# Performance work log

Hardware: AMD Instinct MI355X
Metric: run time of the kernel (lower is better)

## Reference

```python
import jax, jax.numpy as jnp
import numpy as np

NUM_HEADS = 16
EMBED_DIM = 1024
BSZ, T, S = 8, 1024, 1024
NEG_INF = -1e30


def setup_inputs() -> dict:
    key = jax.random.key(0)
    ks = jax.random.split(key, 12)
    E = EMBED_DIM
    decoder_state = jax.random.normal(ks[0], (BSZ, T, E), dtype=jnp.float32)
    source_hids = jax.random.normal(ks[1], (S, BSZ, E), dtype=jnp.float32)
    # realistic padding mask: True = padded position (masked out)
    lengths = jax.random.randint(ks[2], (BSZ,), S // 2, S + 1)
    src_len_mask = jnp.arange(S)[None, :] >= lengths[:, None]  # (BSZ, S) bool
    init = 1.0 / np.sqrt(E)
    Wq = jax.random.uniform(ks[3], (E, E), minval=-init, maxval=init)
    bq = jax.random.uniform(ks[4], (E,), minval=-init, maxval=init)
    Wk = jax.random.uniform(ks[5], (E, E), minval=-init, maxval=init)
    bk = jax.random.uniform(ks[6], (E,), minval=-init, maxval=init)
    Wv = jax.random.uniform(ks[7], (E, E), minval=-init, maxval=init)
    bv = jax.random.uniform(ks[8], (E,), minval=-init, maxval=init)
    Wo = jax.random.uniform(ks[9], (E, E), minval=-init, maxval=init)
    bo = jax.random.uniform(ks[10], (E,), minval=-init, maxval=init)
    return {"decoder_state": decoder_state, "source_hids": source_hids,
            "src_len_mask": src_len_mask, "Wq": Wq, "bq": bq, "Wk": Wk,
            "bk": bk, "Wv": Wv, "bv": bv, "Wo": Wo, "bo": bo}


def reference(decoder_state, source_hids, src_len_mask, Wq, bq, Wk, bk, Wv, bv, Wo, bo):
    B, Tq, E = decoder_state.shape
    Sk = source_hids.shape[0]
    H = NUM_HEADS
    hd = E // H
    scaling = hd ** (-0.5)

    query = jnp.swapaxes(decoder_state, 0, 1)  # (T, B, E)
    q = (query @ Wq.T + bq) * scaling          # (T, B, E)
    k = source_hids @ Wk.T + bk                # (S, B, E)
    v = source_hids @ Wv.T + bv                # (S, B, E)

    q = q.reshape(Tq, B, H, hd)
    k = k.reshape(Sk, B, H, hd)
    v = v.reshape(Sk, B, H, hd)

    scores = jnp.einsum("tbhd,sbhd->bhts", q, k)  # (B, H, T, S)
    scores = jnp.where(src_len_mask[:, None, None, :], NEG_INF, scores)
    weights = jax.nn.softmax(scores, axis=-1)     # (B, H, T, S); dropout p=0

    attn = jnp.einsum("bhts,sbhd->tbhd", weights, v).reshape(Tq, B, E)
    attn = attn @ Wo.T + bo                       # (T, B, E)

    # need_weights: mean over heads -> (B, T, S); then transpose(0,2) -> (S, T, B)
    attn_weights_out = jnp.swapaxes(weights.mean(axis=1), 0, 2)
    # squeeze=True is a no-op here since T != 1
    return attn, attn_weights_out
```

## Files before the change

kernel.cpp:

```cpp
#include <hip/hip_runtime.h>
#include <stdint.h>
#include <stddef.h>

typedef __attribute__((ext_vector_type(8))) short bf16x8;
typedef __attribute__((ext_vector_type(4))) float f32x4;
typedef __attribute__((ext_vector_type(4))) uint32_t u32x4;

#define DEVINL static __device__ __forceinline__

DEVINL float b2f(uint16_t u) {
  uint32_t x = ((uint32_t)u) << 16;
  float f;
  __builtin_memcpy(&f, &x, 4);
  return f;
}

DEVINL uint16_t f2b(float f) {
  uint32_t u;
  __builtin_memcpy(&u, &f, 4);
  return (uint16_t)((u + 0x7fffu + ((u >> 16) & 1u)) >> 16);
}

DEVINL void gload16(const void* gsrc, void* ldst) {
  __builtin_amdgcn_global_load_lds(
      (const __attribute__((address_space(1))) void*)gsrc,
      (__attribute__((address_space(3))) void*)ldst, 16, 0, 0);
}

__global__ void detect_kernel(const void* __restrict__ wq, const void* __restrict__ mask,
                              const void* __restrict__ bq, const void* __restrict__ bk,
                              const void* __restrict__ bv, const void* __restrict__ bo,
                              int* __restrict__ hdr, float* __restrict__ bias) {
  __shared__ int sflag, smask32, slen[8];
  const int tid = threadIdx.x;
  if (tid == 0) { sflag = 0; smask32 = 0; }
  if (tid < 8) slen[tid] = 0;
  __syncthreads();
  const uint16_t* w16 = (const uint16_t*)wq;
  int f = 0;
  for (int i = tid; i < 4096; i += 256) {
    uint16_t u = w16[i];
    uint32_t e = (u >> 7) & 0xFFu;
    if (fabsf(b2f(u)) > 0.25f || e == 0xFFu) f = 1;
  }
  if (f) atomicOr(&sflag, 1);
  const uint8_t* mb = (const uint8_t*)mask;
  int m32 = 0;
  for (int i = tid; i < 8191; i += 256) {
    if ((i & 1023) != 1023 && mb[i] != 0 && mb[i + 1] == 0) m32 = 1;
  }
  if (m32) atomicOr(&smask32, 1);
  __syncthreads();
  if (smask32) {
    const int* mi = (const int*)mask;
    for (int i = tid; i < 8192; i += 256) { if (mi[i] == 0) atomicAdd(&slen[i >> 10], 1); }
  } else {
    for (int i = tid; i < 8192; i += 256) { if (mb[i] == 0) atomicAdd(&slen[i >> 10], 1); }
  }
  __syncthreads();
  if (tid == 0) hdr[0] = sflag;
  if (tid < 8) hdr[1 + tid] = slen[tid];
  const void* bs[4] = {bq, bk, bv, bo};
  for (int j = 0; j < 4; ++j) {
    for (int i = tid; i < 1024; i += 256) {
      float v = sflag ? ((const float*)bs[j])[i] : b2f(((const uint16_t*)bs[j])[i]);
      bias[j * 1024 + i] = v;
    }
  }
}

__global__ __launch_bounds__(256)
void convert_kernel(const void* __restrict__ s0, const void* __restrict__ s1,
                    const void* __restrict__ s2, const void* __restrict__ s3,
                    const void* __restrict__ s4, const void* __restrict__ s5,
                    uint16_t* __restrict__ d0, uint16_t* __restrict__ d1,
                    uint16_t* __restrict__ d2, const int* __restrict__ hdr, int doW) {
  const int isf = hdr[0];
  const size_t n01 = 1048576;
  const size_t nw = 131072;
  const size_t total = doW ? (2 * n01 + 4 * nw) : (2 * n01);
  size_t gid = (size_t)blockIdx.x * 256 + threadIdx.x;
  const size_t stride = (size_t)gridDim.x * 256;
  for (; gid < total; gid += stride) {
    const void* sp;
    uint16_t* dp;
    size_t off;
    if (gid < n01) { sp = s0; dp = d0; off = gid; }
    else if (gid < 2 * n01) { sp = s1; dp = d1; off = gid - n01; }
    else {
      const size_t w = (gid - 2 * n01) >> 17;
      off = (gid - 2 * n01) & (nw - 1);
      sp = (w == 0) ? s2 : (w == 1) ? s3 : (w == 2) ? s4 : s5;
      dp = d2 + w * 1048576;
    }
    if (isf) {
      const float* fp = (const float*)sp + off * 8;
      const f32x4 a = *(const f32x4*)fp;
      const f32x4 c = *(const f32x4*)(fp + 4);
      u32x4 r;
      r[0] = (uint32_t)f2b(a[0]) | ((uint32_t)f2b(a[1]) << 16);
      r[1] = (uint32_t)f2b(a[2]) | ((uint32_t)f2b(a[3]) << 16);
      r[2] = (uint32_t)f2b(c[0]) | ((uint32_t)f2b(c[1]) << 16);
      r[3] = (uint32_t)f2b(c[2]) | ((uint32_t)f2b(c[3]) << 16);
      *(u32x4*)(dp + off * 8) = r;
    } else {
      *(u32x4*)(dp + off * 8) = *(const u32x4*)((const uint16_t*)sp + off * 8);
    }
  }
}

enum { MQ = 0, MK = 1, MV = 2, MO = 3 };

DEVINL u32x4 load8w(const void* __restrict__ src, bool f32, size_t eoff) {
  if (!f32) {
    return *(const u32x4*)((const uint16_t*)src + eoff);
  }
  const float* p = (const float*)src + eoff;
  const f32x4 a = *(const f32x4*)p;
  const f32x4 c = *(const f32x4*)(p + 4);
  u32x4 r;
  r[0] = (uint32_t)f2b(a[0]) | ((uint32_t)f2b(a[1]) << 16);
  r[1] = (uint32_t)f2b(a[2]) | ((uint32_t)f2b(a[3]) << 16);
  r[2] = (uint32_t)f2b(c[0]) | ((uint32_t)f2b(c[1]) << 16);
  r[3] = (uint32_t)f2b(c[2]) | ((uint32_t)f2b(c[3]) << 16);
  return r;
}

__global__ __launch_bounds__(256)
void gemm_qkv(const uint16_t* __restrict__ dec_b, const uint16_t* __restrict__ src_b,
              const void* __restrict__ Wq, const void* __restrict__ Wk,
              const void* __restrict__ Wv, const float* __restrict__ bias,
              const int* __restrict__ hdr, uint16_t* __restrict__ Q,
              uint16_t* __restrict__ K, uint16_t* __restrict__ V, int wIsBf16) {
  __shared__ __align__(16) uint16_t lA[2][8192];
  __shared__ __align__(16) uint16_t lB[2][8192];
  const int tid = threadIdx.x, lane = tid & 63, wave = tid >> 6;
  const int bm = blockIdx.x;
  const int grp = blockIdx.y >> 3, bn = blockIdx.y & 7;
  const int isf = hdr[0];
  const bool wF32 = (wIsBf16 == 0) && (isf != 0);
  const uint16_t* Ab = (grp == 0) ? dec_b : src_b;
  const void* Wr = (grp == 0) ? Wq : (grp == 1) ? Wk : Wv;
  const float* bs = bias + grp * 1024;
  const float scale = (grp == 0) ? 0.125f : 1.f;
  const int wm = wave >> 1, wn = wave & 1;
  const int g = lane >> 4, cc = lane & 15;
  const int lr = lane >> 3, lc = lane & 7;
  const int scc = (lc ^ lr) * 8;

  auto stage = [&](int kt, int buf) {
#pragma unroll
    for (int q = 0; q < 4; ++q) {
      const int j = wave * 4 + q;
      gload16(Ab + (size_t)(bm * 128 + j * 8 + lr) * 1024 + kt * 64 + scc, &lA[buf][j * 512]);
    }
    if (!wF32) {
#pragma unroll
      for (int q = 0; q < 4; ++q) {
        const int j = wave * 4 + q;
        gload16((const uint16_t*)Wr + (size_t)(bn * 128 + j * 8 + lr) * 1024 + kt * 64 + scc, &lB[buf][j * 512]);
      }
    } else {
#pragma unroll
      for (int q = 0; q < 4; ++q) {
        const int j = wave * 4 + q;
        const u32x4 rv = load8w(Wr, true, (size_t)(bn * 128 + j * 8 + lr) * 1024 + kt * 64 + lc * 8);
        *(u32x4*)&lB[buf][j * 512 + lr * 64 + ((lc ^ lr) * 8)] = rv;
      }
    }
  };

  f32x4 acc[4][4];
#pragma unroll
  for (int i = 0; i < 4; ++i)
#pragma unroll
    for (int j = 0; j < 4; ++j) acc[i][j] = (f32x4){0.f, 0.f, 0.f, 0.f};

  stage(0, 0);
  for (int kt = 0; kt < 16; ++kt) {
    const int cur = kt & 1;
    asm volatile("s_waitcnt vmcnt(0) lgkmcnt(0)" ::: "memory");
    __builtin_amdgcn_sched_barrier(0);
    __builtin_amdgcn_s_barrier();
    if (kt + 1 < 16) stage(kt + 1, cur ^ 1);
#pragma unroll
    for (int kk = 0; kk < 2; ++kk) {
      bf16x8 af[4], bfr[4];
#pragma unroll
      for (int mi = 0; mi < 4; ++mi) {
        const int row = wm * 64 + mi * 16 + cc;
        af[mi] = *(const bf16x8*)&lA[cur][row * 64 + (((kk * 4 + g) ^ (cc & 7)) << 3)];
      }
#pragma unroll
      for (int ni = 0; ni < 4; ++ni) {
        const int row = wn * 64 + ni * 16 + cc;
        bfr[ni] = *(const bf16x8*)&lB[cur][row * 64 + (((kk * 4 + g) ^ (cc & 7)) << 3)];
      }
#pragma unroll
      for (int mi = 0; mi < 4; ++mi)
#pragma unroll
        for (int ni = 0; ni < 4; ++ni)
          acc[mi][ni] = __builtin_amdgcn_mfma_f32_16x16x32_bf16(af[mi], bfr[ni], acc[mi][ni], 0, 0, 0);
    }
  }
#pragma unroll
  for (int mi = 0; mi < 4; ++mi) {
#pragma unroll
    for (int ni = 0; ni < 4; ++ni) {
      const int col = bn * 128 + wn * 64 + ni * 16 + cc;
      const float bv = bs[col];
      const int r0 = bm * 128 + wm * 64 + mi * 16 + g * 4;
#pragma unroll
      for (int r = 0; r < 4; ++r) {
        const int row = r0 + r;
        const float v = (acc[mi][ni][r] + bv) * scale;
        if (grp == 0) {
          const int b = row >> 10, t = row & 1023, h = col >> 6, d = col & 63;
          Q[(((size_t)(b * 16 + h) << 10) + t) * 64 + d] = f2b(v);
        } else if (grp == 1) {
          const int s = row >> 3, b = row & 7, h = col >> 6, d = col & 63;
          K[(((size_t)(b * 16 + h) << 10) + s) * 64 + d] = f2b(v);
        } else {
          const int s = row >> 3, b = row & 7, h = col >> 6, d = col & 63;
          V[(((size_t)(b * 16 + h) << 6) + d) * 1024 + s] = f2b(v);
        }
      }
    }
  }
}

template <int MODE>
__global__ __launch_bounds__(256)
void gemm_bt(const uint16_t* __restrict__ Ab, const void* __restrict__ Wr,
             const float* __restrict__ bias, const int* __restrict__ hdr,
             void* __restrict__ outp, float scale, int wIsBf16) {
  __shared__ __align__(16) uint16_t lA[2][8192];
  __shared__ __align__(16) uint16_t lB[2][8192];
  const int tid = threadIdx.x, lane = tid & 63, wave = tid >> 6;
  const int bm = blockIdx.x, bn = blockIdx.y;
  const int isf = hdr[0];
  const bool wF32 = (wIsBf16 == 0) && (isf != 0);
  const int wm = wave >> 1, wn = wave & 1;
  const int g = lane >> 4, cc = lane & 15;
  const int lr = lane >> 3, lc = lane & 7;
  const int scc = (lc ^ lr) * 8;

  auto stage = [&](int kt, int buf) {
#pragma unroll
    for (int q = 0; q < 4; ++q) {
      const int j = wave * 4 + q;
      gload16(Ab + (size_t)(bm * 128 + j * 8 + lr) * 1024 + kt * 64 + scc, &lA[buf][j * 512]);
    }
    if (!wF32) {
#pragma unroll
      for (int q = 0; q < 4; ++q) {
        const int j = wave * 4 + q;
        gload16((const uint16_t*)Wr + (size_t)(bn * 128 + j * 8 + lr) * 1024 + kt * 64 + scc, &lB[buf][j * 512]);
      }
    } else {
#pragma unroll
      for (int q = 0; q < 4; ++q) {
        const int j = wave * 4 + q;
        const u32x4 rv = load8w(Wr, true, (size_t)(bn * 128 + j * 8 + lr) * 1024 + kt * 64 + lc * 8);
        *(u32x4*)&lB[buf][j * 512 + lr * 64 + ((lc ^ lr) * 8)] = rv;
      }
    }
  };

  f32x4 acc[4][4];
#pragma unroll
  for (int i = 0; i < 4; ++i)
#pragma unroll
    for (int j = 0; j < 4; ++j) acc[i][j] = (f32x4){0.f, 0.f, 0.f, 0.f};

  stage(0, 0);
  for (int kt = 0; kt < 16; ++kt) {
    const int cur = kt & 1;
    asm volatile("s_waitcnt vmcnt(0) lgkmcnt(0)" ::: "memory");
    __builtin_amdgcn_sched_barrier(0);
    __builtin_amdgcn_s_barrier();
    if (kt + 1 < 16) stage(kt + 1, cur ^ 1);
#pragma unroll
    for (int kk = 0; kk < 2; ++kk) {
      bf16x8 af[4], bfr[4];
#pragma unroll
      for (int mi = 0; mi < 4; ++mi) {
        const int row = wm * 64 + mi * 16 + cc;
        af[mi] = *(const bf16x8*)&lA[cur][row * 64 + (((kk * 4 + g) ^ (cc & 7)) << 3)];
      }
#pragma unroll
      for (int ni = 0; ni < 4; ++ni) {
        const int row = wn * 64 + ni * 16 + cc;
        bfr[ni] = *(const bf16x8*)&lB[cur][row * 64 + (((kk * 4 + g) ^ (cc & 7)) << 3)];
      }
#pragma unroll
      for (int mi = 0; mi < 4; ++mi)
#pragma unroll
        for (int ni = 0; ni < 4; ++ni)
          acc[mi][ni] = __builtin_amdgcn_mfma_f32_16x16x32_bf16(af[mi], bfr[ni], acc[mi][ni], 0, 0, 0);
    }
  }
#pragma unroll
  for (int mi = 0; mi < 4; ++mi) {
#pragma unroll
    for (int ni = 0; ni < 4; ++ni) {
      const int col = bn * 128 + wn * 64 + ni * 16 + cc;
      const float bv = bias[col];
      const int r0 = bm * 128 + wm * 64 + mi * 16 + g * 4;
#pragma unroll
      for (int r = 0; r < 4; ++r) {
        const int row = r0 + r;
        const float v = (acc[mi][ni][r] + bv) * scale;
        const size_t o = (size_t)row * 1024 + col;
        if (isf) ((float*)outp)[o] = v;
        else ((uint16_t*)outp)[o] = f2b(v);
      }
    }
  }
}

__global__ __launch_bounds__(1024)
void attn_kernel(const uint16_t* __restrict__ Qh, const uint16_t* __restrict__ Kh,
                 const uint16_t* __restrict__ Vh, const int* __restrict__ hdr,
                 uint16_t* __restrict__ AP, uint16_t* __restrict__ Wm) {
  __shared__ __align__(16) uint16_t kbuf[2][8192];
  __shared__ __align__(16) uint16_t vbuf[2][8192];
  __shared__ __align__(16) uint16_t pstash[32][1024];
  __shared__ float pvx[2][32][68];

  const int tid = threadIdx.x, lane = tid & 63, w = tid >> 6;
  const int g = lane >> 4, cc = lane & 15;
  const int wt = w >> 3, ws = w & 7;
  const int dq = (w >> 1) & 3, ks = w & 1;
  const int b = blockIdx.x & 7, tt = blockIdx.x >> 3;
  const int t0 = tt * 32;
  const int len = hdr[1 + b];
  const int tme = tid >> 5, s5 = tid & 31;

  auto stage = [&](int p, int buf) {
    const int hh = p >> 3, st = p & 7;
    const uint16_t* Kb = Kh + ((size_t)(b * 16 + hh) << 16);
    const uint16_t* Vt = Vh + ((size_t)(b * 16 + hh) << 16);
    {
      const int row = tid >> 3;
      const int c = (tid & 7) ^ (row & 7);
      gload16(Kb + (st * 128 + row) * 64 + c * 8, &kbuf[buf][w * 512]);
    }
    {
      const int d = tid >> 4;
      const int c = tid & 15;
      const int cg = (c & 8) | ((c ^ (d & 7)) & 7);
      gload16(Vt + d * 1024 + st * 128 + cg * 8, &vbuf[buf][w * 512]);
    }
  };

  stage(0, 0);

  float wmean[32];
#pragma unroll
  for (int j = 0; j < 32; ++j) wmean[j] = 0.f;

  for (int h = 0; h < 16; ++h) {
    const uint16_t* Qb = Qh + ((size_t)(b * 16 + h) << 16) + (((size_t)(t0 + wt * 16 + cc)) << 6);
    const bf16x8 qf0 = *(const bf16x8*)(Qb + g * 8);
    const bf16x8 qf1 = *(const bf16x8*)(Qb + 32 + g * 8);
    f32x4 pv = (f32x4){0.f, 0.f, 0.f, 0.f};
    for (int st = 0; st < 8; ++st) {
      const int p = h * 8 + st;
      const int cur = p & 1;
      asm volatile("s_waitcnt vmcnt(0)" ::: "memory");
      __builtin_amdgcn_sched_barrier(0);
      __builtin_amdgcn_s_barrier();
      if (p + 1 < 128) stage(p + 1, cur ^ 1);
      {
        const int row = ws * 16 + cc;
        f32x4 a = (f32x4){0.f, 0.f, 0.f, 0.f};
#pragma unroll
        for (int kk = 0; kk < 2; ++kk) {
          const bf16x8 kf = *(const bf16x8*)&kbuf[cur][row * 64 + (((kk * 4 + g) ^ (cc & 7)) << 3)];
          a = __builtin_amdgcn_mfma_f32_16x16x32_bf16(kk ? qf1 : qf0, kf, a, 0, 0, 0);
        }
        const int s = st * 128 + row;
        const bool msk = (s >= len);
        float vv0 = msk ? 0.f : __expf(a[0]);
        float vv1 = msk ? 0.f : __expf(a[1]);
        float vv2 = msk ? 0.f : __expf(a[2]);
        float vv3 = msk ? 0.f : __expf(a[3]);
        uint32_t pk01, pk23;
        asm("v_cvt_pk_bf16_f32 %0, %1, %2" : "=v"(pk01) : "v"(vv0), "v"(vv1));
        asm("v_cvt_pk_bf16_f32 %0, %1, %2" : "=v"(pk23) : "v"(vv2), "v"(vv3));
        const uint16_t pb[4] = {(uint16_t)pk01, (uint16_t)(pk01 >> 16),
                                (uint16_t)pk23, (uint16_t)(pk23 >> 16)};
        const int cbase = st * 16 + ws * 2 + (cc >> 3);
#pragma unroll
        for (int r = 0; r < 4; ++r) {
          const int tl = wt * 16 + g * 4 + r;
          const int cs = (cbase & ~7) | ((cbase ^ tl) & 7);
          pstash[tl][(cs << 3) + (cc & 7)] = pb[r];
        }
      }
      asm volatile("s_waitcnt lgkmcnt(0)" ::: "memory");
      __builtin_amdgcn_sched_barrier(0);
      __builtin_amdgcn_s_barrier();
      {
        const int tr = wt * 16 + cc;
#pragma unroll
        for (int kk = 0; kk < 2; ++kk) {
          const int ca = st * 16 + ks * 8 + kk * 4 + g;
          const int ca2 = (ca & ~7) | ((ca ^ tr) & 7);
          const bf16x8 af = *(const bf16x8*)&pstash[tr][ca2 << 3];
          const int cv = ks * 8 + kk * 4 + g;
          const int cv2 = (cv & 8) | ((cv ^ (cc & 7)) & 7);
          const bf16x8 vf = *(const bf16x8*)&vbuf[cur][(dq * 16 + cc) * 128 + (cv2 << 3)];
          pv = __builtin_amdgcn_mfma_f32_16x16x32_bf16(af, vf, pv, 0, 0, 0);
        }
      }
    }
#pragma unroll
    for (int r = 0; r < 4; ++r)
      pvx[ks][wt * 16 + g * 4 + r][dq * 16 + cc] = pv[r];
    float winv;
    {
      uint32_t p4[16];
#pragma unroll
      for (int q = 0; q < 4; ++q) {
        const int c = s5 + 32 * q;
        const int c2 = (c & ~7) | ((c ^ tme) & 7);
        *(u32x4*)&p4[q * 4] = *(const u32x4*)&pstash[tme][c2 << 3];
      }
      float sm = 0.f;
#pragma unroll
      for (int j = 0; j < 16; ++j) {
        sm += b2f((uint16_t)(p4[j] & 0xffffu));
        sm += b2f((uint16_t)(p4[j] >> 16));
      }
#pragma unroll
      for (int m = 16; m >= 1; m >>= 1) sm += __shfl_xor(sm, m, 64);
      winv = 1.f / sm;
#pragma unroll
      for (int j = 0; j < 16; ++j) {
        wmean[2 * j] += b2f((uint16_t)(p4[j] & 0xffffu)) * winv;
        wmean[2 * j + 1] += b2f((uint16_t)(p4[j] >> 16)) * winv;
      }
    }
    asm volatile("s_waitcnt lgkmcnt(0)" ::: "memory");
    __builtin_amdgcn_sched_barrier(0);
    __builtin_amdgcn_s_barrier();
    {
      const int d0 = s5 * 2;
      const float v0 = (pvx[0][tme][d0] + pvx[1][tme][d0]) * winv;
      const float v1 = (pvx[0][tme][d0 + 1] + pvx[1][tme][d0 + 1]) * winv;
      const uint32_t pk = (uint32_t)f2b(v0) | ((uint32_t)f2b(v1) << 16);
      *(uint32_t*)(AP + ((((size_t)(t0 + tme)) * 8 + b) << 10) + h * 64 + d0) = pk;
    }
  }

  {
    uint16_t* dst = Wm + (((size_t)(b * 1024 + t0 + tme)) << 10);
#pragma unroll
    for (int q = 0; q < 4; ++q) {
      uint16_t ob[8];
#pragma unroll
      for (int e = 0; e < 8; ++e) ob[e] = f2b(wmean[q * 8 + e] * 0.0625f);
      *(u32x4*)(dst + q * 256 + s5 * 8) = *(const u32x4*)ob;
    }
  }
}

__global__ __launch_bounds__(256)
void wtrans_kernel(const uint16_t* __restrict__ Wm, const int* __restrict__ hdr,
                   void* __restrict__ outBase) {
  __shared__ uint16_t lt[8][32][68];
  const int tid = threadIdx.x;
  const int s0 = blockIdx.x * 64, t0 = blockIdx.y * 32;
  const int isf = hdr[0];
  const int rr = tid >> 4;
  const int sc = (tid & 15) * 4;
#pragma unroll
  for (int p = 0; p < 16; ++p) {
    const int row = p * 16 + rr;
    const int b = row >> 5, t = row & 31;
    const uint64_t v = *(const uint64_t*)(Wm + (((size_t)(b * 1024 + t0 + t)) << 10) + s0 + sc);
    *(uint64_t*)&lt[b][t][sc] = v;
  }
  __syncthreads();
#pragma unroll
  for (int p = 0; p < 8; ++p) {
    const int pair = p * 256 + tid;
    const int t = pair & 31, s = pair >> 5;
    const size_t o = 8388608 + ((size_t)(s0 + s) * 1024 + (t0 + t)) * 8;
    if (isf) {
      f32x4 v0, v1;
#pragma unroll
      for (int b = 0; b < 4; ++b) v0[b] = b2f(lt[b][t][s]);
#pragma unroll
      for (int b = 0; b < 4; ++b) v1[b] = b2f(lt[b + 4][t][s]);
      *(f32x4*)((float*)outBase + o) = v0;
      *(f32x4*)((float*)outBase + o + 4) = v1;
    } else {
      u32x4 v;
#pragma unroll
      for (int q = 0; q < 4; ++q)
        v[q] = (uint32_t)lt[2 * q][t][s] | ((uint32_t)lt[2 * q + 1][t][s] << 16);
      *(u32x4*)((uint16_t*)outBase + o) = v;
    }
  }
}

__global__ void fill_pattern(uint32_t* p, size_t n) {
  size_t i = (size_t)blockIdx.x * 256 + threadIdx.x;
  const size_t stride = (size_t)gridDim.x * 256;
  for (; i < n; i += stride) p[i] = 0x3f3f3f3fu;
}

extern "C" void kernel_launch(void* const* d_in, const int* in_sizes, int n_in,
                              void* d_out, int out_size, void* d_ws, size_t ws_size,
                              hipStream_t stream) {
  char* ws = (char*)d_ws;
  int* hdr = (int*)ws;
  float* bias = (float*)(ws + 4096);
  uint16_t* Q = (uint16_t*)(ws + (1u << 20));
  uint16_t* K = Q + 8388608;
  uint16_t* V = K + 8388608;
  uint16_t* AP = V + 8388608;
  uint16_t* Wm = AP + 8388608;
  uint16_t* dec_b = AP;
  uint16_t* src_b = Wm;
  const size_t needBase = (1ull << 20) + 5ull * 16777216ull;
  const size_t needFull = needBase + 8ull * 1048576ull;
  uint16_t* Wb = (uint16_t*)(ws + needBase);
  const int useConvW = (ws_size >= needFull) ? 1 : 0;
  if (ws_size < needBase) {
    fill_pattern<<<1024, 256, 0, stream>>>((uint32_t*)d_out, (size_t)out_size / 2);
    return;
  }

  detect_kernel<<<1, 256, 0, stream>>>(d_in[3], d_in[2], d_in[4], d_in[6], d_in[8], d_in[10], hdr, bias);

  convert_kernel<<<4096, 256, 0, stream>>>(d_in[0], d_in[1], d_in[3], d_in[5], d_in[7], d_in[9],
                                           dec_b, src_b, Wb, hdr, useConvW);

  const void* Wq = useConvW ? (const void*)(Wb + 0 * 1048576) : (const void*)d_in[3];
  const void* Wk = useConvW ? (const void*)(Wb + 1 * 1048576) : (const void*)d_in[5];
  const void* Wv = useConvW ? (const void*)(Wb + 2 * 1048576) : (const void*)d_in[7];
  const void* Wo = useConvW ? (const void*)(Wb + 3 * 1048576) : (const void*)d_in[9];

  gemm_qkv<<<dim3(64, 24), 256, 0, stream>>>(dec_b, src_b, Wq, Wk, Wv, bias, hdr, Q, K, V, useConvW);

  attn_kernel<<<256, 1024, 0, stream>>>(Q, K, V, hdr, AP, Wm);

  wtrans_kernel<<<dim3(16, 32), 256, 0, stream>>>(Wm, hdr, d_out);

  gemm_bt<MO><<<dim3(64, 8), 256, 0, stream>>>(AP, Wo, bias + 3072, hdr, d_out, 1.f, useConvW);
}
```

Measured before the change: 302.1 us.

## Load K and V fragments directly from global memory instead of LDS staging

Drops the double-buffered LDS staging of the K and V tiles and the async global-to-LDS copies. Each wave now reads its K and V MFMA operands straight from global memory into registers. This removes one block-wide barrier and the vmcnt wait per step, and frees about 64 KB of LDS. In exchange, global load latency is no longer hidden behind the previous step, and K/V data is fetched redundantly by several waves, so it relies on cache hits.

```diff
diff --git a/kernel.cpp b/kernel.cpp
--- a/kernel.cpp
+++ b/kernel.cpp
@@ -323,8 +323,6 @@
 void attn_kernel(const uint16_t* __restrict__ Qh, const uint16_t* __restrict__ Kh,
                  const uint16_t* __restrict__ Vh, const int* __restrict__ hdr,
                  uint16_t* __restrict__ AP, uint16_t* __restrict__ Wm) {
-  __shared__ __align__(16) uint16_t kbuf[2][8192];
-  __shared__ __align__(16) uint16_t vbuf[2][8192];
   __shared__ __align__(16) uint16_t pstash[32][1024];
   __shared__ float pvx[2][32][68];
 
@@ -337,49 +335,26 @@
   const int len = hdr[1 + b];
   const int tme = tid >> 5, s5 = tid & 31;
 
-  auto stage = [&](int p, int buf) {
-    const int hh = p >> 3, st = p & 7;
-    const uint16_t* Kb = Kh + ((size_t)(b * 16 + hh) << 16);
-    const uint16_t* Vt = Vh + ((size_t)(b * 16 + hh) << 16);
-    {
-      const int row = tid >> 3;
-      const int c = (tid & 7) ^ (row & 7);
-      gload16(Kb + (st * 128 + row) * 64 + c * 8, &kbuf[buf][w * 512]);
-    }
-    {
-      const int d = tid >> 4;
-      const int c = tid & 15;
-      const int cg = (c & 8) | ((c ^ (d & 7)) & 7);
-      gload16(Vt + d * 1024 + st * 128 + cg * 8, &vbuf[buf][w * 512]);
-    }
-  };
-
-  stage(0, 0);
-
   float wmean[32];
 #pragma unroll
   for (int j = 0; j < 32; ++j) wmean[j] = 0.f;
 
   for (int h = 0; h < 16; ++h) {
     const uint16_t* Qb = Qh + ((size_t)(b * 16 + h) << 16) + (((size_t)(t0 + wt * 16 + cc)) << 6);
+    const uint16_t* Kb = Kh + ((size_t)(b * 16 + h) << 16);
+    const uint16_t* Vt = Vh + ((size_t)(b * 16 + h) << 16);
     const bf16x8 qf0 = *(const bf16x8*)(Qb + g * 8);
     const bf16x8 qf1 = *(const bf16x8*)(Qb + 32 + g * 8);
     f32x4 pv = (f32x4){0.f, 0.f, 0.f, 0.f};
     for (int st = 0; st < 8; ++st) {
-      const int p = h * 8 + st;
-      const int cur = p & 1;
-      asm volatile("s_waitcnt vmcnt(0)" ::: "memory");
-      __builtin_amdgcn_sched_barrier(0);
-      __builtin_amdgcn_s_barrier();
-      if (p + 1 < 128) stage(p + 1, cur ^ 1);
       {
         const int row = ws * 16 + cc;
+        const uint16_t* kp = Kb + (size_t)(st * 128 + row) * 64 + g * 8;
+        const bf16x8 kf0 = *(const bf16x8*)kp;
+        const bf16x8 kf1 = *(const bf16x8*)(kp + 32);
         f32x4 a = (f32x4){0.f, 0.f, 0.f, 0.f};
-#pragma unroll
-        for (int kk = 0; kk < 2; ++kk) {
-          const bf16x8 kf = *(const bf16x8*)&kbuf[cur][row * 64 + (((kk * 4 + g) ^ (cc & 7)) << 3)];
-          a = __builtin_amdgcn_mfma_f32_16x16x32_bf16(kk ? qf1 : qf0, kf, a, 0, 0, 0);
-        }
+        a = __builtin_amdgcn_mfma_f32_16x16x32_bf16(qf0, kf0, a, 0, 0, 0);
+        a = __builtin_amdgcn_mfma_f32_16x16x32_bf16(qf1, kf1, a, 0, 0, 0);
         const int s = st * 128 + row;
         const bool msk = (s >= len);
         float vv0 = msk ? 0.f : __expf(a[0]);
@@ -404,14 +379,13 @@
       __builtin_amdgcn_s_barrier();
       {
         const int tr = wt * 16 + cc;
+        const uint16_t* vp = Vt + (size_t)(dq * 16 + cc) * 1024 + st * 128 + ks * 64 + g * 8;
 #pragma unroll
         for (int kk = 0; kk < 2; ++kk) {
           const int ca = st * 16 + ks * 8 + kk * 4 + g;
           const int ca2 = (ca & ~7) | ((ca ^ tr) & 7);
           const bf16x8 af = *(const bf16x8*)&pstash[tr][ca2 << 3];
-          const int cv = ks * 8 + kk * 4 + g;
-          const int cv2 = (cv & 8) | ((cv ^ (cc & 7)) & 7);
-          const bf16x8 vf = *(const bf16x8*)&vbuf[cur][(dq * 16 + cc) * 128 + (cv2 << 3)];
+          const bf16x8 vf = *(const bf16x8*)(vp + kk * 32);
           pv = __builtin_amdgcn_mfma_f32_16x16x32_bf16(af, vf, pv, 0, 0, 0);
         }
       }
```

Result: slower. 466.5 us (+54.4%).
